# Kernel optimization log

Measured on AMD Instinct MI355X. Metric: run time of the kernel, lower is better.

## Reference

```python
import jax, jax.numpy as jnp
import numpy as np

ALPHA = 0.2  # LeakyReLU negative slope
NEG_INF = -9e15


def setup_inputs() -> dict:
    key = jax.random.key(0)
    ks = jax.random.split(key, 9)
    B, N, Fin, Fout, H = 4, 1024, 256, 256, 32
    h = jax.random.normal(ks[0], (B, N, Fin), dtype=jnp.float32)
    mz = jax.random.uniform(ks[1], (B, N, 1), dtype=jnp.float32) * 2000.0
    adj = jax.random.randint(ks[2], (B, N, N), 0, 2, dtype=jnp.int32)
    # xavier_uniform with gain=1.414
    def xavier(k, shape, gain=1.414):
        fan_in, fan_out = shape[0], shape[1]
        bound = gain * np.sqrt(6.0 / (fan_in + fan_out))
        return jax.random.uniform(k, shape, jnp.float32, -bound, bound)
    W = xavier(ks[3], (Fin, Fout))
    a = xavier(ks[4], (2 * Fout, 1))
    w1 = xavier(ks[5], (1, H), gain=1.0)
    b1 = jnp.zeros((H,), jnp.float32)
    w2 = xavier(ks[6], (H, 1), gain=1.0)
    b2 = jnp.zeros((1,), jnp.float32)
    return {"h": h, "mz": mz, "W": W, "a": a, "w1": w1, "b1": b1, "w2": w2, "b2": b2, "adj": adj}


def reference(h, mz, W, a, w1, b1, w2, b2, adj):
    # h: (B,N,Fin), mz: (B,N,1), adj: (B,N,N)
    Wh = jnp.matmul(h, W)                       # (B,N,Fout)
    Fout = W.shape[1]
    a1 = a[:Fout, 0]                            # (Fout,)
    a2 = a[Fout:, 0]                            # (Fout,)
    # e[b,i,j] = leaky_relu(Wh[b,i]@a1 + Wh[b,j]@a2)  (identical to concat trick)
    s1 = jnp.einsum('bnf,f->bn', Wh, a1)
    s2 = jnp.einsum('bnf,f->bn', Wh, a2)
    e = jax.nn.leaky_relu(s1[:, :, None] + s2[:, None, :], negative_slope=ALPHA)  # (B,N,N)
    # |mz_i - mz_j| with first row/col zeroed
    diff = jnp.abs(mz - jnp.swapaxes(mz, 1, 2))  # (B,N,N)
    diff = diff.at[:, 0, :].set(0.0)
    diff = diff.at[:, :, 0].set(0.0)
    # tiny per-edge MLP: Linear(1,32)->ReLU->Linear(32,1)
    hdn = jax.nn.relu(diff[..., None] * w1[0] + b1)       # (B,N,N,32)
    diff_term = jnp.einsum('bijh,h->bij', hdn, w2[:, 0]) + b2[0]
    e = e + diff_term
    att = jnp.where(adj > 0, e, NEG_INF)
    att = jax.nn.softmax(att, axis=2)
    # dropout is identity in eval mode
    h_prime = jnp.matmul(att, Wh)               # (B,N,Fout)
    return jax.nn.elu(h_prime)
```

## Files before the change

### kernel.cpp

```cpp
#include <hip/hip_runtime.h>
#include <hip/hip_bf16.h>

#define ALPHA 0.2f
#define NEGINF -9000000000000000.0f

typedef __attribute__((ext_vector_type(8))) short short8;
typedef __attribute__((ext_vector_type(4))) float f32x4;
typedef __attribute__((ext_vector_type(4))) int i32x4;
typedef __attribute__((ext_vector_type(4))) unsigned short u16x4;

static constexpr int NB = 4, NN = 1024, NF = 256, NH = 32;

__device__ __forceinline__ unsigned short f2bf(float x) {
  union { float f; unsigned u; } v; v.f = x;
  unsigned r = v.u + 0x7fffu + ((v.u >> 16) & 1u);
  return (unsigned short)(r >> 16);
}

__global__ __launch_bounds__(256) void prep_kernel(
    const float* __restrict__ W, const float* __restrict__ a,
    const int* __restrict__ adj, float* __restrict__ wa1,
    float* __restrict__ wa2, unsigned short* __restrict__ WTp,
    unsigned long long* __restrict__ adjm) {
  int k = blockIdx.x;
  int t = threadIdx.x;
  const int* ap = adj + ((size_t)(k * 16 + (t >> 4))) * NN + (t & 15) * 64;
  i32x4 av[16];
#pragma unroll
  for (int i = 0; i < 16; ++i) av[i] = *(const i32x4*)(ap + i * 4);

  float w = W[k * NF + t];
  WTp[(((k >> 3) * NF) + t) * 8 + (k & 7)] = f2bf(w);
  float p1 = w * a[t];
  float p2 = w * a[NF + t];
#pragma unroll
  for (int off = 32; off >= 1; off >>= 1) {
    p1 += __shfl_xor(p1, off);
    p2 += __shfl_xor(p2, off);
  }
  __shared__ float r1[4], r2[4];
  if ((t & 63) == 0) { r1[t >> 6] = p1; r2[t >> 6] = p2; }
  __syncthreads();
  if (t == 0) {
    wa1[k] = r1[0] + r1[1] + r1[2] + r1[3];
    wa2[k] = r2[0] + r2[1] + r2[2] + r2[3];
  }

  unsigned long long m = 0ull;
#pragma unroll
  for (int i = 0; i < 16; ++i)
#pragma unroll
    for (int u = 0; u < 4; ++u)
      m |= (unsigned long long)(av[i][u] > 0) << (i * 4 + u);
  adjm[(size_t)k * 256 + t] = m;
}

__global__ __launch_bounds__(512) void wh_kernel(
    const float* __restrict__ h, const unsigned short* __restrict__ WTp,
    const float* __restrict__ wa1, const float* __restrict__ wa2,
    unsigned short* __restrict__ WhP, float* __restrict__ s1g,
    float* __restrict__ s2g) {
  __shared__ unsigned short hs[16 * 256];
  int bid = blockIdx.x;
  int b = bid >> 6;
  int rb = (bid & 63) << 4;
  int t = threadIdx.x;
  {
    int row = t >> 5, c0 = (t & 31) * 8;
    const float* src = h + (size_t)(b * NN + rb + row) * NF + c0;
    f32x4 v0 = *(const f32x4*)src;
    f32x4 v1 = *(const f32x4*)(src + 4);
    unsigned short tmp[8] = {f2bf(v0.x), f2bf(v0.y), f2bf(v0.z), f2bf(v0.w),
                             f2bf(v1.x), f2bf(v1.y), f2bf(v1.z), f2bf(v1.w)};
    int off = row * 512 + ((c0 * 2) ^ ((row & 7) << 4));
    *(short8*)((char*)hs + off) = *(const short8*)tmp;
    f32x4 a10 = *(const f32x4*)(wa1 + c0);
    f32x4 a11 = *(const f32x4*)(wa1 + c0 + 4);
    f32x4 a20 = *(const f32x4*)(wa2 + c0);
    f32x4 a21 = *(const f32x4*)(wa2 + c0 + 4);
    float d1 = v0.x * a10.x + v0.y * a10.y + v0.z * a10.z + v0.w * a10.w +
               v1.x * a11.x + v1.y * a11.y + v1.z * a11.z + v1.w * a11.w;
    float d2 = v0.x * a20.x + v0.y * a20.y + v0.z * a20.z + v0.w * a20.w +
               v1.x * a21.x + v1.y * a21.y + v1.z * a21.z + v1.w * a21.w;
#pragma unroll
    for (int off2 = 16; off2 >= 1; off2 >>= 1) {
      d1 += __shfl_xor(d1, off2);
      d2 += __shfl_xor(d2, off2);
    }
    if ((t & 31) == 0) {
      s1g[b * NN + rb + row] = d1;
      s2g[b * NN + rb + row] = d2;
    }
  }
  __syncthreads();
  int wid = t >> 6, lane = t & 63;
  int fb = wid * 32;
  int rowa = lane & 15, kg = lane >> 4;
  f32x4 acc0 = {0.f, 0.f, 0.f, 0.f}, acc1 = {0.f, 0.f, 0.f, 0.f};
#pragma unroll
  for (int ks = 0; ks < 8; ++ks) {
    int k0 = ks * 32;
    short8 af = *(const short8*)((const char*)hs + rowa * 512 +
                                 ((2 * (k0 + kg * 8)) ^ ((rowa & 7) << 4)));
    int kc = ks * 4 + kg;
    short8 bf0 = *(const short8*)(WTp + ((kc * NF) + fb + (lane & 15)) * 8);
    short8 bf1 = *(const short8*)(WTp + ((kc * NF) + fb + 16 + (lane & 15)) * 8);
    acc0 = __builtin_amdgcn_mfma_f32_16x16x32_bf16(af, bf0, acc0, 0, 0, 0);
    acc1 = __builtin_amdgcn_mfma_f32_16x16x32_bf16(af, bf1, acc1, 0, 0, 0);
  }
#pragma unroll
  for (int r = 0; r < 4; ++r) {
    int jl = (lane >> 4) * 4 + r;
    int j = rb + jl;
    int base = ((b << 7) + (j >> 3)) * NF;
    WhP[(size_t)(base + fb + (lane & 15)) * 8 + (j & 7)] = f2bf(acc0[r]);
    WhP[(size_t)(base + fb + 16 + (lane & 15)) * 8 + (j & 7)] = f2bf(acc1[r]);
  }
}

__global__ __launch_bounds__(512) void attn_kernel(
    const float* __restrict__ mz, const unsigned long long* __restrict__ adjm,
    const unsigned short* __restrict__ WhP,
    const float* __restrict__ w1, const float* __restrict__ b1,
    const float* __restrict__ w2, const float* __restrict__ b2,
    const float* __restrict__ s1g, const float* __restrict__ s2g,
    float* __restrict__ out) {
  __shared__ unsigned short Pb[32 * 1024];
  __shared__ unsigned long long adjmsh[32][16];
  __shared__ float mzs[1024];
  __shared__ float s2s[1024];
  __shared__ float s1s[32];
  __shared__ float rinv[32];
  __shared__ float segsh[3];

  int bid0 = blockIdx.x;
  int bid = (bid0 & 7) * 32 + (bid0 >> 3);
  int b = bid >> 6;
  int rg = (bid >> 1) & 31;
  int fh = bid & 1;
  int rb = rg << 5;
  int fbw_base = fh << 7;
  int t = threadIdx.x;
  int wid = t >> 6, lane = t & 63;

  int fbw = fbw_base + wid * 16;
  int fl = lane & 15, kg = lane >> 4;
  const unsigned short* whb = WhP + (((size_t)b) << 7) * NF * 8;
  short8 pf[36];
#pragma unroll
  for (int ks = 0; ks < 8; ++ks)
    pf[ks] =
        *(const short8*)(whb + (size_t)(((ks * 4 + kg) * NF) + fbw + fl) * 8);

  if (t < 512) {
    int r = t >> 4, sg = t & 15;
    adjmsh[r][sg] = adjm[(size_t)(b * NN + rb + r) * 16 + sg];
  }
  if (t < NH) {
    float w1h = w1[t], b1h = b1[t], w2h = w2[t];
    bool bp = (w1h != 0.f) && (b1h != 0.f) && ((b1h > 0.f) != (w1h > 0.f));
    bool act = (w1h + b1h) > 0.f;
    float cA = act ? w2h * w1h : 0.f;
    float cB = act ? w2h * b1h : 0.f;
    float nbp = bp ? 1.f : 0.f;
#pragma unroll
    for (int off = 16; off >= 1; off >>= 1) {
      cA += __shfl_xor(cA, off);
      cB += __shfl_xor(cB, off);
      nbp += __shfl_xor(nbp, off);
    }
    if (t == 0) {
      segsh[0] = (nbp == 0.f) ? 1.f : 0.f;
      segsh[1] = cA;
      segsh[2] = cB + b2[0];
    }
  }
  for (int i = t; i < NN; i += 512) {
    mzs[i] = mz[b * NN + i];
    s2s[i] = s2g[b * NN + i];
  }
  if (t < 32) s1s[t] = s1g[b * NN + rb + t];
  __syncthreads();

  float segF = segsh[0], segA = segsh[1], segB = segsh[2];
  float b2v = b2[0];
  for (int rr = 0; rr < 4; ++rr) {
    int row = wid * 4 + rr;
    int ig = rb + row;
    float s1v = s1s[row];
    float mzi = mzs[ig];
    float segA_r = (ig == 0) ? 0.f : segA;
    float e[16];
    if (segF != 0.f) {
#pragma unroll
      for (int c = 0; c < 4; ++c) {
        int j0 = c * 256 + lane * 4;
        unsigned nib =
            (unsigned)(adjmsh[row][c * 4 + (lane >> 4)] >> ((lane & 15) * 4)) &
            0xFu;
        f32x4 mzv = *(const f32x4*)(mzs + j0);
        f32x4 s2v = *(const f32x4*)(s2s + j0);
#pragma unroll
        for (int u = 0; u < 4; ++u) {
          float s = s1v + s2v[u];
          float dd = mzi - mzv[u];
          float ee = fmaxf(s, 0.f) +
                     fmaf(ALPHA, fminf(s, 0.f),
                          fmaf(fabsf(dd), segA_r, segB));
          e[c * 4 + u] = (nib & (1u << u)) ? ee : NEGINF;
        }
      }
      if (lane == 0 && ig != 0) {
        float s = s1v + s2s[0];
        float ee = fmaxf(s, 0.f) + fmaf(ALPHA, fminf(s, 0.f), segB);
        e[0] = ((unsigned)(adjmsh[row][0]) & 1u) ? ee : NEGINF;
      }
    } else {
#pragma unroll
      for (int c = 0; c < 4; ++c) {
        int j0 = c * 256 + lane * 4;
        unsigned nib =
            (unsigned)(adjmsh[row][c * 4 + (lane >> 4)] >> ((lane & 15) * 4)) &
            0xFu;
        f32x4 mzv = *(const f32x4*)(mzs + j0);
        f32x4 s2v = *(const f32x4*)(s2s + j0);
        float d[4], acc[4];
#pragma unroll
        for (int u = 0; u < 4; ++u) {
          float dd = fabsf(mzi - mzv[u]);
          d[u] = (ig == 0 || (j0 + u) == 0) ? 0.f : dd;
          acc[u] = b2v;
        }
#pragma unroll 1
        for (int hh = 0; hh < NH; ++hh) {
          float w1h = w1[hh], b1h = b1[hh], w2h = w2[hh];
#pragma unroll
          for (int u = 0; u < 4; ++u)
            acc[u] += fmaxf(d[u] * w1h + b1h, 0.f) * w2h;
        }
#pragma unroll
        for (int u = 0; u < 4; ++u) {
          float s = s1v + s2v[u];
          s = s > 0.f ? s : ALPHA * s;
          e[c * 4 + u] = (nib & (1u << u)) ? (s + acc[u]) : NEGINF;
        }
      }
    }
    float m01 = fmaxf(fmaxf(e[0], e[1]), e[2]);
    float m02 = fmaxf(fmaxf(e[3], e[4]), e[5]);
    float m03 = fmaxf(fmaxf(e[6], e[7]), e[8]);
    float m04 = fmaxf(fmaxf(e[9], e[10]), e[11]);
    float m05 = fmaxf(fmaxf(e[12], e[13]), e[14]);
    float m = fmaxf(fmaxf(fmaxf(m01, m02), fmaxf(m03, m04)),
                    fmaxf(m05, e[15]));
#pragma unroll
    for (int off = 32; off >= 1; off >>= 1) m = fmaxf(m, __shfl_xor(m, off));
    float sum = 0.f;
#pragma unroll
    for (int q = 0; q < 16; ++q) {
      e[q] = __expf(e[q] - m);
      sum += e[q];
    }
#pragma unroll
    for (int off = 32; off >= 1; off >>= 1) sum += __shfl_xor(sum, off);
#pragma unroll
    for (int c = 0; c < 4; ++c) {
      u16x4 pk = {f2bf(e[c * 4 + 0]), f2bf(e[c * 4 + 1]),
                  f2bf(e[c * 4 + 2]), f2bf(e[c * 4 + 3])};
      int byteoff = row * 2048 + ((512 * c + 8 * lane) ^ ((row & 7) << 4));
      *(u16x4*)((char*)Pb + byteoff) = pk;
    }
    if (lane == 0) rinv[row] = 1.0f / sum;
  }
  __syncthreads();

  {
    f32x4 acc0 = {0.f, 0.f, 0.f, 0.f}, acc1 = {0.f, 0.f, 0.f, 0.f};
    int abase = fl * 2048;
#pragma unroll
    for (int ks = 0; ks < 32; ++ks) {
      if (ks + 8 < 32)
        pf[ks + 8] = *(const short8*)(
            whb + (size_t)((((ks + 8) * 4 + kg) * NF) + fbw + fl) * 8);
      int aoff = (2 * (ks * 32 + kg * 8)) ^ ((fl & 7) << 4);
      short8 af0 = *(const short8*)((const char*)Pb + abase + aoff);
      short8 af1 = *(const short8*)((const char*)Pb + abase + 32768 + aoff);
      acc0 = __builtin_amdgcn_mfma_f32_16x16x32_bf16(af0, pf[ks], acc0, 0, 0, 0);
      acc1 = __builtin_amdgcn_mfma_f32_16x16x32_bf16(af1, pf[ks], acc1, 0, 0, 0);
    }
#pragma unroll
    for (int r = 0; r < 4; ++r) {
      int il0 = (lane >> 4) * 4 + r;
      int il1 = il0 + 16;
      float x0 = acc0[r] * rinv[il0];
      float x1 = acc1[r] * rinv[il1];
      x0 = x0 > 0.f ? x0 : (__expf(x0) - 1.f);
      x1 = x1 > 0.f ? x1 : (__expf(x1) - 1.f);
      out[(size_t)(b * NN + rb + il0) * NF + fbw + fl] = x0;
      out[(size_t)(b * NN + rb + il1) * NF + fbw + fl] = x1;
    }
  }
}

extern "C" void kernel_launch(void* const* d_in, const int* in_sizes, int n_in,
                              void* d_out, int out_size, void* d_ws, size_t ws_size,
                              hipStream_t stream) {
  const float* h   = (const float*)d_in[0];
  const float* mz  = (const float*)d_in[1];
  const float* W   = (const float*)d_in[2];
  const float* a   = (const float*)d_in[3];
  const float* w1  = (const float*)d_in[4];
  const float* b1  = (const float*)d_in[5];
  const float* w2  = (const float*)d_in[6];
  const float* b2  = (const float*)d_in[7];
  const int*   adj = (const int*)d_in[8];
  float* out = (float*)d_out;

  unsigned short* WTp = (unsigned short*)d_ws;
  unsigned short* WhP = WTp + 65536;
  float* wa1 = (float*)(WhP + (size_t)NB * NN * NF);
  float* wa2 = wa1 + 256;
  float* s1g = wa2 + 256;
  float* s2g = s1g + NB * NN;
  unsigned long long* adjm = (unsigned long long*)(s2g + NB * NN);

  prep_kernel<<<dim3(256), dim3(256), 0, stream>>>(W, a, adj, wa1, wa2, WTp,
                                                   adjm);
  wh_kernel<<<dim3(256), dim3(512), 0, stream>>>(h, WTp, wa1, wa2, WhP, s1g, s2g);
  attn_kernel<<<dim3(256), dim3(512), 0, stream>>>(mz, adjm, WhP, w1, b1, w2,
                                                   b2, s1g, s2g, out);
}
```

Before: 26.47 us.

## Split attention into 16-row blocks of 256 threads and drop register prefetch

The attention kernel now handles 16 query rows per block with 4 waves instead of 32 rows with 8 waves, doubling the grid to 512 blocks. The P·Wh matmul is restructured so each wave covers 32 output features for the 16 rows with one A fragment, and the 36-register B prefetch array is replaced by direct global loads inside an 8-way unrolled loop. The goal is to cut LDS and register use per block for better occupancy and to fill all CUs. In exchange, each block recomputes the shared per-batch loads and global B loads are no longer prefetched ahead of the MFMAs.

Result: slower. 29.25 us (+10.5%).

```diff
diff --git a/kernel.cpp b/kernel.cpp
--- a/kernel.cpp
+++ b/kernel.cpp
@@ -118,41 +118,32 @@
   }
 }
 
-__global__ __launch_bounds__(512) void attn_kernel(
+__global__ __launch_bounds__(256) void attn_kernel(
     const float* __restrict__ mz, const unsigned long long* __restrict__ adjm,
     const unsigned short* __restrict__ WhP,
     const float* __restrict__ w1, const float* __restrict__ b1,
     const float* __restrict__ w2, const float* __restrict__ b2,
     const float* __restrict__ s1g, const float* __restrict__ s2g,
     float* __restrict__ out) {
-  __shared__ unsigned short Pb[32 * 1024];
-  __shared__ unsigned long long adjmsh[32][16];
+  __shared__ unsigned short Pb[16 * 1024];
+  __shared__ unsigned long long adjmsh[16][16];
   __shared__ float mzs[1024];
   __shared__ float s2s[1024];
-  __shared__ float s1s[32];
-  __shared__ float rinv[32];
+  __shared__ float s1s[16];
+  __shared__ float rinv[16];
   __shared__ float segsh[3];
 
   int bid0 = blockIdx.x;
-  int bid = (bid0 & 7) * 32 + (bid0 >> 3);
-  int b = bid >> 6;
-  int rg = (bid >> 1) & 31;
+  int bid = (bid0 & 7) * 64 + (bid0 >> 3);
+  int b = bid >> 7;
+  int rg = (bid >> 1) & 63;
   int fh = bid & 1;
-  int rb = rg << 5;
+  int rb = rg << 4;
   int fbw_base = fh << 7;
   int t = threadIdx.x;
   int wid = t >> 6, lane = t & 63;
 
-  int fbw = fbw_base + wid * 16;
-  int fl = lane & 15, kg = lane >> 4;
-  const unsigned short* whb = WhP + (((size_t)b) << 7) * NF * 8;
-  short8 pf[36];
-#pragma unroll
-  for (int ks = 0; ks < 8; ++ks)
-    pf[ks] =
-        *(const short8*)(whb + (size_t)(((ks * 4 + kg) * NF) + fbw + fl) * 8);
-
-  if (t < 512) {
+  {
     int r = t >> 4, sg = t & 15;
     adjmsh[r][sg] = adjm[(size_t)(b * NN + rb + r) * 16 + sg];
   }
@@ -175,11 +166,11 @@
       segsh[2] = cB + b2[0];
     }
   }
-  for (int i = t; i < NN; i += 512) {
+  for (int i = t; i < NN; i += 256) {
     mzs[i] = mz[b * NN + i];
     s2s[i] = s2g[b * NN + i];
   }
-  if (t < 32) s1s[t] = s1g[b * NN + rb + t];
+  if (t < 16) s1s[t] = s1g[b * NN + rb + t];
   __syncthreads();
 
   float segF = segsh[0], segA = segsh[1], segB = segsh[2];
@@ -275,29 +266,33 @@
   __syncthreads();
 
   {
+    int fb = fbw_base + wid * 32;
+    int rowa = lane & 15, kg = lane >> 4;
+    const unsigned short* whb = WhP + (((size_t)b) << 7) * NF * 8;
     f32x4 acc0 = {0.f, 0.f, 0.f, 0.f}, acc1 = {0.f, 0.f, 0.f, 0.f};
-    int abase = fl * 2048;
-#pragma unroll
+#pragma unroll 8
     for (int ks = 0; ks < 32; ++ks) {
-      if (ks + 8 < 32)
-        pf[ks + 8] = *(const short8*)(
-            whb + (size_t)((((ks + 8) * 4 + kg) * NF) + fbw + fl) * 8);
-      int aoff = (2 * (ks * 32 + kg * 8)) ^ ((fl & 7) << 4);
-      short8 af0 = *(const short8*)((const char*)Pb + abase + aoff);
-      short8 af1 = *(const short8*)((const char*)Pb + abase + 32768 + aoff);
-      acc0 = __builtin_amdgcn_mfma_f32_16x16x32_bf16(af0, pf[ks], acc0, 0, 0, 0);
-      acc1 = __builtin_amdgcn_mfma_f32_16x16x32_bf16(af1, pf[ks], acc1, 0, 0, 0);
+      int k0 = ks * 32;
+      short8 af = *(const short8*)((const char*)Pb + rowa * 2048 +
+                                   ((2 * (k0 + kg * 8)) ^ ((rowa & 7) << 4)));
+      int kc = ks * 4 + kg;
+      short8 bf0 = *(const short8*)(whb + (size_t)((kc * NF) + fb + rowa) * 8);
+      short8 bf1 =
+          *(const short8*)(whb + (size_t)((kc * NF) + fb + 16 + rowa) * 8);
+      acc0 = __builtin_amdgcn_mfma_f32_16x16x32_bf16(af, bf0, acc0, 0, 0, 0);
+      acc1 = __builtin_amdgcn_mfma_f32_16x16x32_bf16(af, bf1, acc1, 0, 0, 0);
     }
 #pragma unroll
     for (int r = 0; r < 4; ++r) {
-      int il0 = (lane >> 4) * 4 + r;
-      int il1 = il0 + 16;
-      float x0 = acc0[r] * rinv[il0];
-      float x1 = acc1[r] * rinv[il1];
+      int il = (lane >> 4) * 4 + r;
+      float inv = rinv[il];
+      float x0 = acc0[r] * inv;
+      float x1 = acc1[r] * inv;
       x0 = x0 > 0.f ? x0 : (__expf(x0) - 1.f);
       x1 = x1 > 0.f ? x1 : (__expf(x1) - 1.f);
-      out[(size_t)(b * NN + rb + il0) * NF + fbw + fl] = x0;
-      out[(size_t)(b * NN + rb + il1) * NF + fbw + fl] = x1;
+      size_t ob = (size_t)(b * NN + rb + il) * NF + fb + rowa;
+      out[ob] = x0;
+      out[ob + 16] = x1;
     }
   }
 }
@@ -327,6 +322,6 @@
   prep_kernel<<<dim3(256), dim3(256), 0, stream>>>(W, a, adj, wa1, wa2, WTp,
                                                    adjm);
   wh_kernel<<<dim3(256), dim3(512), 0, stream>>>(h, WTp, wa1, wa2, WhP, s1g, s2g);
-  attn_kernel<<<dim3(256), dim3(512), 0, stream>>>(mz, adjm, WhP, w1, b1, w2,
+  attn_kernel<<<dim3(512), dim3(256), 0, stream>>>(mz, adjm, WhP, w1, b1, w2,
                                                    b2, s1g, s2g, out);
 }
```
